# Kernel optimization log

Measured on AMD Instinct MI355X. Metric: run time of the kernel, lower is better.

Reference implementation:

```python
import jax, jax.numpy as jnp
import numpy as np

N = 100000   # nodes
E = 1200000  # directed edges
F_IN, HID, EMB = 5, 64, 16

def setup_inputs() -> dict:
    key = jax.random.key(0)
    ks = jax.random.split(key, 12)
    # node features: [lambda, mu, is_comp, is_AND, is_OR]
    lam = jax.random.uniform(ks[0], (N, 1), jnp.float32) * 0.01
    mu = jax.random.uniform(ks[1], (N, 1), jnp.float32) * 0.1
    node_type = jax.random.randint(ks[2], (N,), 0, 3)
    onehot = jax.nn.one_hot(node_type, 3, dtype=jnp.float32)
    x = jnp.concatenate([lam, mu, onehot], axis=1)  # [N,5]
    edge_index = jax.random.randint(ks[3], (2, E), 0, N, dtype=jnp.int32)

    def lin(k, fi, fo):
        s = 1.0 / np.sqrt(fi)
        return jax.random.uniform(k, (fi, fo), jnp.float32, -s, s)

    return {
        "x": x, "edge_index": edge_index,
        "T": jnp.float32(100.0), "T_max": jnp.float32(500.0),
        "W1": lin(ks[4], F_IN, HID), "b1": jnp.zeros((HID,), jnp.float32),
        "W2": lin(ks[5], HID, HID), "b2": jnp.zeros((HID,), jnp.float32),
        "W3": lin(ks[6], HID, EMB), "b3": jnp.zeros((EMB,), jnp.float32),
        "P1": lin(ks[7], EMB + 8, 64), "pb1": jnp.zeros((64,), jnp.float32),
        "P2": lin(ks[8], 64, 32), "pb2": jnp.zeros((32,), jnp.float32),
        "P3": lin(ks[9], 32, 4), "pb3": jnp.zeros((4,), jnp.float32),
    }

def gcn_conv(h_in, src, dst, W, b):
    """PyG GCNConv: add self-loops, symmetric D^-1/2 (A+I) D^-1/2 norm."""
    h = h_in @ W  # [N,F]
    # degree with self-loops: 1 + in-degree (count on target nodes)
    deg = jax.ops.segment_sum(jnp.ones((E,), jnp.float32), dst, num_segments=N) + 1.0
    dinv = jax.lax.rsqrt(deg)  # [N]
    norm = dinv[src] * dinv[dst]  # [E]
    agg = jax.ops.segment_sum(h[src] * norm[:, None], dst, num_segments=N)
    agg = agg + h * (dinv * dinv)[:, None]  # self-loop term norm = 1/deg
    return agg + b

def reference(x, edge_index, T, T_max, W1, b1, W2, b2, W3, b3,
              P1, pb1, P2, pb2, P3, pb3):
    src, dst = edge_index[0], edge_index[1]
    h = jax.nn.relu(gcn_conv(x, src, dst, W1, b1))
    h = jax.nn.relu(gcn_conv(h, src, dst, W2, b2))
    h = gcn_conv(h, src, dst, W3, b3)
    embedding = jnp.mean(h, axis=0, keepdims=True)  # global_mean_pool, batch=0 -> [1,EMB]

    T_norm = T / T_max
    comp = x[:, 2]
    n_comp = jnp.sum(comp)
    n_AND = jnp.sum(x[:, 3])
    n_OR = jnp.sum(x[:, 4])
    safe = jnp.maximum(n_comp, 1.0)
    has = n_comp > 0
    avg_lambda = jnp.where(has, jnp.sum(x[:, 0] * comp) / safe, 0.0)
    avg_mu = jnp.where(has, jnp.sum(x[:, 1] * comp) / safe, 0.0)
    t_inv = 1.0 / (1.0 + T_norm)
    gf = jnp.stack([n_comp, n_AND, n_OR, n_AND + n_OR,
                    avg_lambda, avg_mu, T_norm * 50.0, t_inv * 50.0])[None, :]  # [1,8]

    emb = jnp.concatenate([embedding, gf], axis=1)  # [1,24]
    hmlp = jax.nn.relu(emb @ P1 + pb1)
    hmlp = jax.nn.relu(hmlp @ P2 + pb2)
    raw = hmlp @ P3 + pb3  # [1,4]

    val = jax.nn.softplus(raw + 2.0)
    alpha_min = 1.0 + val[:, 0]
    alpha_max = alpha_min + val[:, 1] + 0.5
    beta_min = 1.0 + val[:, 2]
    beta_max = beta_min + val[:, 3] + 0.5
    out = jnp.stack([alpha_min, alpha_max, beta_min, beta_max], axis=1)  # [1,4]
    return out, emb
```

## Files before the change

kernel.cpp:

```cpp
#include <hip/hip_runtime.h>

#define NN 100000
#define NE 1200000
#define NB_SCAN ((NN + 255) / 256)

__global__ void k_hist(const int* __restrict__ ei, int* __restrict__ cnt) {
    int i = blockIdx.x * 256 + threadIdx.x;
    if (i < NE) atomicAdd(&cnt[ei[NE + i]], 1);
}

__global__ void k_scan_block(const int* __restrict__ cnt, int* __restrict__ incl,
                             int* __restrict__ bsum, float* __restrict__ dinv) {
    __shared__ int s[256];
    int t = threadIdx.x;
    int i = blockIdx.x * 256 + t;
    int v = (i < NN) ? cnt[i] : 0;
    if (i < NN) dinv[i] = rsqrtf((float)v + 1.0f);
    s[t] = v;
    __syncthreads();
    for (int off = 1; off < 256; off <<= 1) {
        int add = (t >= off) ? s[t - off] : 0;
        __syncthreads();
        s[t] += add;
        __syncthreads();
    }
    if (i < NN) incl[i] = s[t];
    if (t == 255) bsum[blockIdx.x] = s[255];
}

__global__ void k_scan_bsum(int* __restrict__ bsum) {
    __shared__ int s[512];
    int t = threadIdx.x;
    s[t] = (t < NB_SCAN) ? bsum[t] : 0;
    __syncthreads();
    for (int off = 1; off < 512; off <<= 1) {
        int add = (t >= off) ? s[t - off] : 0;
        __syncthreads();
        s[t] += add;
        __syncthreads();
    }
    if (t < NB_SCAN) bsum[t] = s[t];
}

__global__ void k_scan_add(const int* __restrict__ cnt, const int* __restrict__ incl,
                           const int* __restrict__ bsum, int* __restrict__ rowptr) {
    int i = blockIdx.x * 256 + threadIdx.x;
    if (i >= NN) return;
    int base = (blockIdx.x > 0) ? bsum[blockIdx.x - 1] : 0;
    rowptr[i] = base + incl[i] - cnt[i];
    if (i == 0) rowptr[NN] = NE;
}

__global__ void k_scatter(const int* __restrict__ ei, const int* __restrict__ rowptr,
                          int* __restrict__ cursor, int* __restrict__ srcs) {
    int e = blockIdx.x * 256 + threadIdx.x;
    if (e >= NE) return;
    int dst = ei[NE + e];
    int pos = rowptr[dst] + atomicAdd(&cursor[dst], 1);
    srcs[pos] = ei[e];
}

__global__ void k_lin_first(const float* __restrict__ x, const float* __restrict__ W,
                            float* __restrict__ h) {
    __shared__ float Ws[5 * 64];
    int t = threadIdx.x;
    for (int i = t; i < 320; i += 256) Ws[i] = W[i];
    __syncthreads();
    int r = t >> 6, c = t & 63;
    int row = blockIdx.x * 4 + r;
    if (row >= NN) return;
    float acc = 0.f;
#pragma unroll
    for (int k = 0; k < 5; k++) acc += x[row * 5 + k] * Ws[k * 64 + c];
    h[(size_t)row * 64 + c] = acc;
}

__global__ void k_lin64(const float* __restrict__ in, const float* __restrict__ W,
                        float* __restrict__ h) {
    __shared__ float Ws[64 * 64];
    __shared__ float rows[256];
    int t = threadIdx.x;
    for (int i = t; i < 4096; i += 256) Ws[i] = W[i];
    int base = blockIdx.x * 4;
    int gidx = base * 64 + t;
    rows[t] = (gidx < NN * 64) ? in[gidx] : 0.f;
    __syncthreads();
    int r = t >> 6, c = t & 63, row = base + r;
    if (row >= NN) return;
    float acc = 0.f;
#pragma unroll
    for (int k = 0; k < 64; k++) acc += rows[r * 64 + k] * Ws[k * 64 + c];
    h[(size_t)row * 64 + c] = acc;
}

__global__ void k_lin3(const float* __restrict__ in, const float* __restrict__ W,
                       float* __restrict__ h) {
    __shared__ float Ws[64 * 16];
    __shared__ float rows[16 * 64];
    int t = threadIdx.x;
    for (int i = t; i < 1024; i += 256) Ws[i] = W[i];
    int base = blockIdx.x * 16;
    for (int i = t; i < 1024; i += 256) {
        int g = base * 64 + i;
        rows[i] = (g < NN * 64) ? in[g] : 0.f;
    }
    __syncthreads();
    int r = t >> 4, c = t & 15, row = base + r;
    if (row >= NN) return;
    float acc = 0.f;
#pragma unroll
    for (int k = 0; k < 64; k++) acc += rows[r * 64 + k] * Ws[k * 16 + c];
    h[(size_t)row * 16 + c] = acc;
}

template <bool RELU>
__global__ void k_agg64(const int* __restrict__ rowptr, const int* __restrict__ srcs,
                        const float* __restrict__ dinv, const float* __restrict__ h,
                        const float* __restrict__ b, float* __restrict__ out) {
    int t = threadIdx.x;
    int n = blockIdx.x * 4 + (t >> 6);
    if (n >= NN) return;
    int c = t & 63;
    int e0 = rowptr[n], e1 = rowptr[n + 1];
    float dvn = dinv[n];
    float acc0 = 0.f, acc1 = 0.f, acc2 = 0.f, acc3 = 0.f;
    int j = e0;
    for (; j + 3 < e1; j += 4) {
        int s0 = srcs[j], s1 = srcs[j + 1], s2 = srcs[j + 2], s3 = srcs[j + 3];
        float w0 = dinv[s0], w1 = dinv[s1], w2 = dinv[s2], w3 = dinv[s3];
        acc0 += h[(size_t)s0 * 64 + c] * w0;
        acc1 += h[(size_t)s1 * 64 + c] * w1;
        acc2 += h[(size_t)s2 * 64 + c] * w2;
        acc3 += h[(size_t)s3 * 64 + c] * w3;
    }
    for (; j < e1; j++) {
        int s0 = srcs[j];
        acc0 += h[(size_t)s0 * 64 + c] * dinv[s0];
    }
    float v = ((acc0 + acc1) + (acc2 + acc3)) * dvn
            + h[(size_t)n * 64 + c] * dvn * dvn + b[c];
    if (RELU) v = fmaxf(v, 0.f);
    out[(size_t)n * 64 + c] = v;
}

__global__ void k_agg16_reduce(const int* __restrict__ rowptr, const int* __restrict__ srcs,
                               const float* __restrict__ dinv, const float* __restrict__ h,
                               const float* __restrict__ b, float* __restrict__ red) {
    int t = threadIdx.x;
    int lane = t & 63, wv = t >> 6;
    int c = lane & 15, slot = lane >> 4;
    int gw = blockIdx.x * 4 + wv;
    int nw = gridDim.x * 4;
    float acc = 0.f;
    for (int n = gw; n < NN; n += nw) {
        int e0 = rowptr[n], e1 = rowptr[n + 1];
        float dvn = dinv[n];
        float es = 0.f;
        for (int j = e0 + slot; j < e1; j += 4) {
            int s0 = srcs[j];
            es += h[(size_t)s0 * 16 + c] * dinv[s0];
        }
        es += __shfl_xor(es, 16, 64);
        es += __shfl_xor(es, 32, 64);
        if (slot == 0)
            acc += es * dvn + h[(size_t)n * 16 + c] * dvn * dvn + b[c];
    }
    __shared__ float s[4][16];
    if (slot == 0) s[wv][c] = acc;
    __syncthreads();
    if (t < 16) atomicAdd(&red[t], (s[0][t] + s[1][t]) + (s[2][t] + s[3][t]));
}

__global__ void k_reduce_gf(const float* __restrict__ x, float* __restrict__ red) {
    int t = threadIdx.x;
    float sc = 0, sa = 0, so = 0, sl = 0, sm = 0;
    for (int i = blockIdx.x * 256 + t; i < NN; i += gridDim.x * 256) {
        float lam = x[i * 5 + 0], mu = x[i * 5 + 1];
        float c = x[i * 5 + 2], a = x[i * 5 + 3], o = x[i * 5 + 4];
        sc += c; sa += a; so += o; sl += lam * c; sm += mu * c;
    }
    __shared__ float s[256];
    float vals[5] = {sc, sa, so, sl, sm};
#pragma unroll
    for (int k = 0; k < 5; k++) {
        s[t] = vals[k];
        __syncthreads();
        for (int off = 128; off > 0; off >>= 1) {
            if (t < off) s[t] += s[t + off];
            __syncthreads();
        }
        if (t == 0) atomicAdd(&red[16 + k], s[0]);
        __syncthreads();
    }
}

__device__ __forceinline__ float softplus_f(float x) {
    return (x > 20.f) ? x : log1pf(expf(x));
}

__global__ void k_mlp(const float* __restrict__ red,
                      const float* __restrict__ T, const float* __restrict__ Tmax,
                      const float* __restrict__ P1, const float* __restrict__ pb1,
                      const float* __restrict__ P2, const float* __restrict__ pb2,
                      const float* __restrict__ P3, const float* __restrict__ pb3,
                      float* __restrict__ out) {
    __shared__ float emb[24];
    __shared__ float hm1[64];
    __shared__ float hm2[32];
    __shared__ float val[4];
    int t = threadIdx.x;
    if (t < 16) emb[t] = red[t] / (float)NN;
    if (t == 0) {
        float sc = red[16], sa = red[17], so = red[18], sl = red[19], sm = red[20];
        float Tn = T[0] / Tmax[0];
        emb[16] = sc;
        emb[17] = sa;
        emb[18] = so;
        emb[19] = sa + so;
        float safe = fmaxf(sc, 1.0f);
        bool has = sc > 0.f;
        emb[20] = has ? sl / safe : 0.f;
        emb[21] = has ? sm / safe : 0.f;
        emb[22] = Tn * 50.f;
        emb[23] = (1.f / (1.f + Tn)) * 50.f;
    }
    __syncthreads();
    {
        float acc = pb1[t];
#pragma unroll
        for (int k = 0; k < 24; k++) acc += emb[k] * P1[k * 64 + t];
        hm1[t] = fmaxf(acc, 0.f);
    }
    __syncthreads();
    if (t < 32) {
        float acc = pb2[t];
#pragma unroll
        for (int k = 0; k < 64; k++) acc += hm1[k] * P2[k * 32 + t];
        hm2[t] = fmaxf(acc, 0.f);
    }
    __syncthreads();
    if (t < 4) {
        float acc = pb3[t];
#pragma unroll
        for (int k = 0; k < 32; k++) acc += hm2[k] * P3[k * 4 + t];
        val[t] = softplus_f(acc + 2.0f);
    }
    __syncthreads();
    if (t == 0) {
        float amin = 1.f + val[0];
        float amax = amin + val[1] + 0.5f;
        float bmin = 1.f + val[2];
        float bmax = bmin + val[3] + 0.5f;
        out[0] = amin; out[1] = amax; out[2] = bmin; out[3] = bmax;
    }
    if (t >= 4 && t < 28) out[t] = emb[t - 4];
}

extern "C" void kernel_launch(void* const* d_in, const int* in_sizes, int n_in,
                              void* d_out, int out_size, void* d_ws, size_t ws_size,
                              hipStream_t stream) {
    const float* x    = (const float*)d_in[0];
    const int*   ei   = (const int*)d_in[1];
    const float* T    = (const float*)d_in[2];
    const float* Tmax = (const float*)d_in[3];
    const float* W1   = (const float*)d_in[4];
    const float* b1   = (const float*)d_in[5];
    const float* W2   = (const float*)d_in[6];
    const float* b2   = (const float*)d_in[7];
    const float* W3   = (const float*)d_in[8];
    const float* b3   = (const float*)d_in[9];
    const float* P1   = (const float*)d_in[10];
    const float* pb1  = (const float*)d_in[11];
    const float* P2   = (const float*)d_in[12];
    const float* pb2  = (const float*)d_in[13];
    const float* P3   = (const float*)d_in[14];
    const float* pb3  = (const float*)d_in[15];
    float* out = (float*)d_out;

    char* w = (char*)d_ws;
    float* bufH   = (float*)w;                 w += (size_t)NN * 64 * 4;
    float* bufA   = (float*)w;                 w += (size_t)NN * 64 * 4;
    int*   cnt    = (int*)w;                   w += (size_t)NN * 4;
    int*   cursor = (int*)w;                   w += (size_t)NN * 4;
    float* red    = (float*)w;                 w += 32 * 4;
    float* dinv   = (float*)w;                 w += (size_t)NN * 4;
    int*   incl   = (int*)w;                   w += (size_t)NN * 4;
    int*   rowptr = (int*)w;                   w += (size_t)(NN + 1) * 4;
    int*   srcs   = (int*)w;                   w += (size_t)NE * 4;
    int*   bsum   = (int*)w;                   w += 512 * 4;

    hipMemsetAsync(cnt, 0, (2 * (size_t)NN + 32) * sizeof(int), stream);

    k_hist<<<(NE + 255) / 256, 256, 0, stream>>>(ei, cnt);
    k_scan_block<<<NB_SCAN, 256, 0, stream>>>(cnt, incl, bsum, dinv);
    k_scan_bsum<<<1, 512, 0, stream>>>(bsum);
    k_scan_add<<<NB_SCAN, 256, 0, stream>>>(cnt, incl, bsum, rowptr);
    k_scatter<<<(NE + 255) / 256, 256, 0, stream>>>(ei, rowptr, cursor, srcs);

    k_lin_first<<<(NN + 3) / 4, 256, 0, stream>>>(x, W1, bufH);
    k_agg64<true><<<(NN + 3) / 4, 256, 0, stream>>>(rowptr, srcs, dinv, bufH, b1, bufA);

    k_lin64<<<(NN + 3) / 4, 256, 0, stream>>>(bufA, W2, bufH);
    k_agg64<true><<<(NN + 3) / 4, 256, 0, stream>>>(rowptr, srcs, dinv, bufH, b2, bufA);

    k_lin3<<<(NN + 15) / 16, 256, 0, stream>>>(bufA, W3, bufH);
    k_agg16_reduce<<<2048, 256, 0, stream>>>(rowptr, srcs, dinv, bufH, b3, red);

    k_reduce_gf<<<1024, 256, 0, stream>>>(x, red);
    k_mlp<<<1, 64, 0, stream>>>(red, T, Tmax, P1, pb1, P2, pb2, P3, pb3, out);
}
```

Measured before the change: 564.7 us.

## Aggregate raw 5-dim features before first linear layer; window the CSR scatter

For the first GCN layer, neighbor aggregation now runs on the 5-wide input features, and the 5x64 weight, bias and ReLU are applied afterwards. This relies on linearity and replaces a 64-wide gather per edge with a 5-wide one. The CSR scatter is also split into 8 node-range windows, each pass rescanning all edges, so that atomics and writes land in a narrower address range. The cost is 8 reads of the destination array and an extra small intermediate buffer.

```diff
diff --git a/kernel.cpp b/kernel.cpp
--- a/kernel.cpp
+++ b/kernel.cpp
@@ -3,6 +3,9 @@
 #define NN 100000
 #define NE 1200000
 #define NB_SCAN ((NN + 255) / 256)
+#define NPASS 8
+#define WNODES ((NN + NPASS - 1) / NPASS)
+#define EB 128
 
 __global__ void k_hist(const int* __restrict__ ei, int* __restrict__ cnt) {
     int i = blockIdx.x * 256 + threadIdx.x;
@@ -51,28 +54,59 @@
     if (i == 0) rowptr[NN] = NE;
 }
 
-__global__ void k_scatter(const int* __restrict__ ei, const int* __restrict__ rowptr,
-                          int* __restrict__ cursor, int* __restrict__ srcs) {
-    int e = blockIdx.x * 256 + threadIdx.x;
-    if (e >= NE) return;
-    int dst = ei[NE + e];
-    int pos = rowptr[dst] + atomicAdd(&cursor[dst], 1);
-    srcs[pos] = ei[e];
-}
-
-__global__ void k_lin_first(const float* __restrict__ x, const float* __restrict__ W,
-                            float* __restrict__ h) {
+__global__ void k_scatter_win(const int* __restrict__ ei, const int* __restrict__ rowptr,
+                              int* __restrict__ cursor, int* __restrict__ srcs) {
+    int pass = blockIdx.x / EB;
+    int blk  = blockIdx.x % EB;
+    int lo = pass * WNODES;
+    int hi = lo + WNODES;
+    for (int e = blk * 256 + threadIdx.x; e < NE; e += EB * 256) {
+        int dst = ei[NE + e];
+        if (dst >= lo && dst < hi) {
+            int pos = rowptr[dst] + atomicAdd(&cursor[dst], 1);
+            srcs[pos] = ei[e];
+        }
+    }
+}
+
+__global__ void k_aggx(const int* __restrict__ rowptr, const int* __restrict__ srcs,
+                       const float* __restrict__ dinv, const float* __restrict__ x,
+                       float* __restrict__ aggx) {
+    int t = threadIdx.x;
+    int n = blockIdx.x * 4 + (t >> 6);
+    if (n >= NN) return;
+    int lane = t & 63, c = lane & 7, slot = lane >> 3;
+    int e0 = rowptr[n], e1 = rowptr[n + 1];
+    float es = 0.f;
+    if (c < 5) {
+        for (int j = e0 + slot; j < e1; j += 8) {
+            int s = srcs[j];
+            es += x[(size_t)s * 5 + c] * dinv[s];
+        }
+    }
+    es += __shfl_xor(es, 8, 64);
+    es += __shfl_xor(es, 16, 64);
+    es += __shfl_xor(es, 32, 64);
+    float dvn = dinv[n];
+    if (slot == 0 && c < 5)
+        aggx[(size_t)n * 5 + c] = es * dvn + x[(size_t)n * 5 + c] * dvn * dvn;
+}
+
+__global__ void k_lin_first(const float* __restrict__ aggx, const float* __restrict__ W,
+                            const float* __restrict__ b, float* __restrict__ h) {
     __shared__ float Ws[5 * 64];
+    __shared__ float bs[64];
     int t = threadIdx.x;
     for (int i = t; i < 320; i += 256) Ws[i] = W[i];
+    if (t < 64) bs[t] = b[t];
     __syncthreads();
     int r = t >> 6, c = t & 63;
     int row = blockIdx.x * 4 + r;
     if (row >= NN) return;
-    float acc = 0.f;
-#pragma unroll
-    for (int k = 0; k < 5; k++) acc += x[row * 5 + k] * Ws[k * 64 + c];
-    h[(size_t)row * 64 + c] = acc;
+    float acc = bs[c];
+#pragma unroll
+    for (int k = 0; k < 5; k++) acc += aggx[(size_t)row * 5 + k] * Ws[k * 64 + c];
+    h[(size_t)row * 64 + c] = fmaxf(acc, 0.f);
 }
 
 __global__ void k_lin64(const float* __restrict__ in, const float* __restrict__ W,
@@ -288,6 +322,7 @@
     int*   rowptr = (int*)w;                   w += (size_t)(NN + 1) * 4;
     int*   srcs   = (int*)w;                   w += (size_t)NE * 4;
     int*   bsum   = (int*)w;                   w += 512 * 4;
+    float* aggx   = (float*)w;                 w += (size_t)NN * 5 * 4;
 
     hipMemsetAsync(cnt, 0, (2 * (size_t)NN + 32) * sizeof(int), stream);
 
@@ -295,10 +330,10 @@
     k_scan_block<<<NB_SCAN, 256, 0, stream>>>(cnt, incl, bsum, dinv);
     k_scan_bsum<<<1, 512, 0, stream>>>(bsum);
     k_scan_add<<<NB_SCAN, 256, 0, stream>>>(cnt, incl, bsum, rowptr);
-    k_scatter<<<(NE + 255) / 256, 256, 0, stream>>>(ei, rowptr, cursor, srcs);
-
-    k_lin_first<<<(NN + 3) / 4, 256, 0, stream>>>(x, W1, bufH);
-    k_agg64<true><<<(NN + 3) / 4, 256, 0, stream>>>(rowptr, srcs, dinv, bufH, b1, bufA);
+    k_scatter_win<<<NPASS * EB, 256, 0, stream>>>(ei, rowptr, cursor, srcs);
+
+    k_aggx<<<(NN + 3) / 4, 256, 0, stream>>>(rowptr, srcs, dinv, x, aggx);
+    k_lin_first<<<(NN + 3) / 4, 256, 0, stream>>>(aggx, W1, b1, bufA);
 
     k_lin64<<<(NN + 3) / 4, 256, 0, stream>>>(bufA, W2, bufH);
     k_agg64<true><<<(NN + 3) / 4, 256, 0, stream>>>(rowptr, srcs, dinv, bufH, b2, bufA);
```

After: 506.5 us. -10.3%, faster.
